# Kernel tuning notes

Measured on AMD Instinct MI355X. Metric: run time of the kernel, lower is better.

The kernel has to match this reference:

```python
import jax, jax.numpy as jnp
import numpy as np
from jax import lax

WINDOW_SIZE = 11
CHANNEL = 3
SIGMA = 1.5


def _build_window():
    # 1D gaussian, normalized, then outer product -> (C, 1, k, k) depthwise kernel
    coords = jnp.arange(WINDOW_SIZE, dtype=jnp.float32) - WINDOW_SIZE // 2
    g = jnp.exp(-coords ** 2 / (2.0 * SIGMA ** 2))
    g = g / g.sum()
    w2d = jnp.outer(g, g)  # (k, k)
    return jnp.broadcast_to(w2d[None, None], (CHANNEL, 1, WINDOW_SIZE, WINDOW_SIZE))


def _dwconv(x, w):
    pad = WINDOW_SIZE // 2
    return lax.conv_general_dilated(
        x, w,
        window_strides=(1, 1),
        padding=[(pad, pad), (pad, pad)],
        dimension_numbers=("NCHW", "OIHW", "NCHW"),
        feature_group_count=CHANNEL,
    )


def setup_inputs() -> dict:
    key = jax.random.key(0)
    k1, k2 = jax.random.split(key)
    pred = jax.random.uniform(k1, (16, 3, 512, 512), dtype=jnp.float32)
    target = jax.random.uniform(k2, (16, 3, 512, 512), dtype=jnp.float32)
    return {"pred": pred, "target": target}


def reference(pred, target):
    C1, C2 = 0.01 ** 2, 0.03 ** 2
    w = _build_window().astype(pred.dtype)

    mu_x = _dwconv(pred, w)
    mu_y = _dwconv(target, w)
    mu_x_sq = mu_x * mu_x
    mu_y_sq = mu_y * mu_y
    mu_xy = mu_x * mu_y

    sg_x = _dwconv(pred * pred, w) - mu_x_sq
    sg_y = _dwconv(target * target, w) - mu_y_sq
    sg_xy = _dwconv(pred * target, w) - mu_xy

    ssim_map = ((2.0 * mu_xy + C1) * (2.0 * sg_xy + C2)) / (
        (mu_x_sq + mu_y_sq + C1) * (sg_x + sg_y + C2)
    )
    return 1.0 - ssim_map.mean()
```

## Files before the change

### kernel.cpp

```cpp
#include <hip/hip_runtime.h>


namespace {
constexpr int IMG   = 512;
constexpr int NCH   = 48;
constexpr int TW    = 64;
constexpr int TH    = 32;
constexpr int WR    = 44;
constexpr int WC    = 80;
constexpr int SLOTS = WC / 4;
constexpr int TSLOT = WR * SLOTS;
constexpr int NSL   = 2 * TSLOT;
constexpr int TPX   = IMG / TW;
constexpr int TPY   = IMG / TH;
constexpr int NBLK  = TPX * TPY * NCH;
constexpr int NPART = NBLK * 4;
constexpr int RS    = 48;
constexpr int SXN   = WR * WC;

constexpr float Wf[11] = {
    0.00102838f, 0.00759876f, 0.03600077f, 0.10936069f, 0.21300554f,
    0.26601172f,
    0.21300554f, 0.10936069f, 0.03600077f, 0.00759876f, 0.00102838f };

constexpr float band_wc(int d) {
    return (d >= 0 && d < 11) ? Wf[d] : 0.f;
}

constexpr unsigned short f2h(float f) {
    if (f == 0.f) return 0;
    unsigned u = __builtin_bit_cast(unsigned, f);
    int  he = int((u >> 23) & 0xff) - 127 + 15;
    unsigned hm   = (u & 0x7fffff) >> 13;
    unsigned rest = u & 0x1fff;
    if (rest > 0x1000 || (rest == 0x1000 && (hm & 1))) ++hm;
    return (unsigned short)((unsigned(he) << 10) + hm);
}

struct Tabs { unsigned short a[64][8]; unsigned short b[64][8]; };
constexpr Tabs build_tabs() {
    Tabs t{};
    for (int lane = 0; lane < 64; ++lane) {
        const int nr = lane & 15, quad = lane >> 4;
        for (int jj = 0; jj < 8; ++jj) {
            const int k = quad * 8 + jj;
            t.a[lane][jj] = f2h(band_wc(k - nr));
            t.b[lane][jj] = f2h(band_wc(k - nr - 3));
        }
    }
    return t;
}
}

__device__ __constant__ __align__(16) Tabs g_tabs = build_tabs();

typedef _Float16 half8 __attribute__((ext_vector_type(8)));
typedef _Float16 half4v __attribute__((ext_vector_type(4)));
typedef _Float16 h2 __attribute__((ext_vector_type(2)));
typedef float float4v __attribute__((ext_vector_type(4)));
typedef float float2v __attribute__((ext_vector_type(2)));

__device__ inline h2 pk(float a, float b) {
    auto v = __builtin_amdgcn_cvt_pkrtz(a, b);
    h2 r;
    __builtin_memcpy(&r, &v, sizeof(r));
    return r;
}

union H8 { half8 v; h2 p[4]; };

__device__ __forceinline__ void gl2l(const float* g, void* l) {
    __builtin_amdgcn_global_load_lds(
        (const __attribute__((address_space(1))) unsigned int*)g,
        (__attribute__((address_space(3))) unsigned int*)l, 16, 0, 0);
}

__global__ __launch_bounds__(256, 4) void ssim_tile_kernel(
    const float* __restrict__ pred, const float* __restrict__ tgt,
    float* __restrict__ partial)
{
    __shared__ __align__(16) float sx[2 * SXN];
    __shared__ __align__(16) _Float16 sc[4][2][16][RS];

    const int t    = threadIdx.x;
    const int w    = t >> 6;
    const int lane = t & 63;
    const int nr   = lane & 15;
    const int quad = lane >> 4;

    const int bid  = blockIdx.x;
    const int img  = bid >> 7;
    const int tile = bid & 127;
    const int tx   = (tile & 7) * TW;
    const int ty   = (tile >> 3) * TH;

    const float* __restrict__ p = pred + (size_t)img * (IMG * IMG);
    const float* __restrict__ q = tgt  + (size_t)img * (IMG * IMG);

    #pragma unroll
    for (int i = 0; i < 7; ++i) {
        const int j = i * 4 + w;
        const int L = j * 64 + lane;
        if (L < NSL) {
            const int tens = (L >= TSLOT) ? 1 : 0;
            const int Lt   = L - tens * TSLOT;
            const int row  = Lt / SLOTS;
            const int sp   = Lt - row * SLOTS;
            int sl = sp - (row & 7);
            if (sl < 0) sl += SLOTS;
            const int gy   = min(max(ty - 5 + row, 0), IMG - 1);
            const int gx   = min(max(tx - 8 + 4 * sl, 0), IMG - 4);
            const float* src = (tens ? q : p) + gy * IMG + gx;
            gl2l(src, (char*)sx + (size_t)j * 1024);
        }
    }
    __syncthreads();

    const half8 Aband = *(const half8*)(g_tabs.a[lane]);
    const half8 Bband = *(const half8*)(g_tabs.b[lane]);
    const float4v zf = {0.f, 0.f, 0.f, 0.f};
    const half8 z8 = {};

    constexpr float C1 = 1e-4f, C2 = 9e-4f;
    const float2v C1v = {C1, C1};
    const float2v C2v = {C2, C2};
    const float2v K12 = {C1 + C2, C1 + C2};
    float2v lsum2 = {0.f, 0.f};

    {
        const int c = w;
        const bool okc_ = ((unsigned)(tx + 16 * c - 8 + 8 * quad)
                           <= (unsigned)(IMG - 8));

        half8 fx[3], fy[3];
        #pragma unroll
        for (int s = 0; s < 3; ++s) {
            const int row  = 16 * s + nr;
            const int rowr = min(row, WR - 1);
            const bool ok  = okc_ && (row < WR) &&
                             ((unsigned)(ty - 5 + row) < (unsigned)IMG);
            const int sl0 = 4 * c + 2 * quad;
            const int r7  = rowr & 7;
            int pos0 = sl0 + r7;     if (pos0 >= SLOTS) pos0 -= SLOTS;
            int pos1 = sl0 + 1 + r7; if (pos1 >= SLOTS) pos1 -= SLOTS;
            const float* b0 = sx + rowr * WC;
            const float* b1 = b0 + SXN;
            float4 xA = *(const float4*)(b0 + 4 * pos0);
            float4 xB = *(const float4*)(b0 + 4 * pos1);
            float4 yA = *(const float4*)(b1 + 4 * pos0);
            float4 yB = *(const float4*)(b1 + 4 * pos1);
            H8 ax, ay;
            ax.p[0] = pk(xA.x, xA.y); ax.p[1] = pk(xA.z, xA.w);
            ax.p[2] = pk(xB.x, xB.y); ax.p[3] = pk(xB.z, xB.w);
            ay.p[0] = pk(yA.x, yA.y); ay.p[1] = pk(yA.z, yA.w);
            ay.p[2] = pk(yB.x, yB.y); ay.p[3] = pk(yB.z, yB.w);
            if (!ok) { ax.v = z8; ay.v = z8; }
            fx[s] = ax.v;
            fy[s] = ay.v;
        }

        auto hw = [&](int slot, int s, float4v d) {
            h2 lo = pk(d[0], d[1]);
            h2 hi = pk(d[2], d[3]);
            half4v hh = {lo[0], lo[1], hi[0], hi[1]};
            *(half4v*)&sc[w][slot][nr][16 * s + 4 * quad] = hh;
        };
        auto rdv = [&](int slot, int pb) -> half8 {
            return *(const half8*)&sc[w][slot][nr][pb + 8 * quad];
        };
        #define HMA(a) __builtin_amdgcn_mfma_f32_16x16x32_f16((a), Bband, zf, 0, 0, 0)
        #define VMA(b) __builtin_amdgcn_mfma_f32_16x16x32_f16(Aband, (b), zf, 0, 0, 0)

        float4v a0[5], a1[5];
        #pragma unroll
        for (int s = 0; s < 3; ++s) { hw(0, s, HMA(fx[s])); hw(1, s, HMA(fy[s])); }
        a0[0] = VMA(rdv(0, 0));  a1[0] = VMA(rdv(0, 16));
        a0[1] = VMA(rdv(1, 0));  a1[1] = VMA(rdv(1, 16));
        #pragma unroll
        for (int s = 0; s < 3; ++s) { hw(0, s, HMA(fx[s] * fx[s])); hw(1, s, HMA(fy[s] * fy[s])); }
        a0[2] = VMA(rdv(0, 0));  a1[2] = VMA(rdv(0, 16));
        a0[3] = VMA(rdv(1, 0));  a1[3] = VMA(rdv(1, 16));
        #pragma unroll
        for (int s = 0; s < 3; ++s) { hw(0, s, HMA(fx[s] * fy[s])); }
        a0[4] = VMA(rdv(0, 0));  a1[4] = VMA(rdv(0, 16));

        #pragma unroll
        for (int v = 0; v < 2; ++v) {
            const float4v* A = v ? a1 : a0;
            #pragma unroll
            for (int h = 0; h < 2; ++h) {
                float2v mx  = {A[0][2*h], A[0][2*h+1]};
                float2v my  = {A[1][2*h], A[1][2*h+1]};
                float2v ex2 = {A[2][2*h], A[2][2*h+1]};
                float2v ey2 = {A[3][2*h], A[3][2*h+1]};
                float2v exy = {A[4][2*h], A[4][2*h+1]};
                float2v P  = mx * my;
                float2v U  = mx * mx + my * my + C1v;
                float2v n1 = 2.f * P + C1v;
                float2v n2 = 2.f * (exy - P) + C2v;
                float2v num = n1 * n2;
                float2v e1 = (ex2 + ey2) - U + K12;
                float2v den = U * e1;
                float2v r = {__builtin_amdgcn_rcpf(den.x),
                             __builtin_amdgcn_rcpf(den.y)};
                lsum2 += num * r;
            }
        }
        #undef HMA
        #undef VMA
    }

    float lsum = lsum2.x + lsum2.y;
    #pragma unroll
    for (int off = 32; off > 0; off >>= 1)
        lsum += __shfl_down(lsum, off, 64);
    if (lane == 0) partial[(bid << 2) + w] = lsum;
}

__global__ __launch_bounds__(1024) void ssim_finish(
    const float* __restrict__ partial, float* __restrict__ out)
{
    __shared__ float wred[16];
    const int t = threadIdx.x;
    float s = 0.f;
    #pragma unroll
    for (int i = 0; i < NPART / 1024; ++i)
        s += partial[t + i * 1024];
    #pragma unroll
    for (int off = 32; off > 0; off >>= 1)
        s += __shfl_down(s, off, 64);
    if ((t & 63) == 0) wred[t >> 6] = s;
    __syncthreads();
    if (t == 0) {
        float acc = 0.f;
        #pragma unroll
        for (int i = 0; i < 16; ++i) acc += wred[i];
        out[0] = 1.f - acc * (1.f / (float)((long long)NCH * IMG * IMG));
    }
}

extern "C" void kernel_launch(void* const* d_in, const int* in_sizes, int n_in,
                              void* d_out, int out_size, void* d_ws, size_t ws_size,
                              hipStream_t stream)
{
    const float* pred = (const float*)d_in[0];
    const float* tgt  = (const float*)d_in[1];
    float* out     = (float*)d_out;
    float* partial = (float*)d_ws;

    ssim_tile_kernel<<<NBLK, 256, 0, stream>>>(pred, tgt, partial);
    ssim_finish<<<1, 1024, 0, stream>>>(partial, out);
}
```

Before: 127.8 us.

## Process four tiles per block with double-buffered async LDS staging

Each block now walks a vertical strip of four 64x32 tiles instead of one. While one LDS buffer is being computed, the global-to-LDS loads for the next tile go into a second buffer, synchronised with explicit vmcnt waits and barriers. This is meant to hide global load latency behind MFMA work and to cut block-launch overhead. The scratch buffer becomes a single slot reused in sequence, which serialises the horizontal and vertical passes. Doubled LDS use and the lowered launch bound cut occupancy, and halo rows are still reloaded for every tile.

```diff
diff --git a/kernel.cpp b/kernel.cpp
--- a/kernel.cpp
+++ b/kernel.cpp
@@ -6,14 +6,15 @@
 constexpr int NCH   = 48;
 constexpr int TW    = 64;
 constexpr int TH    = 32;
+constexpr int NT    = 4;
 constexpr int WR    = 44;
 constexpr int WC    = 80;
 constexpr int SLOTS = WC / 4;
 constexpr int TSLOT = WR * SLOTS;
 constexpr int NSL   = 2 * TSLOT;
 constexpr int TPX   = IMG / TW;
-constexpr int TPY   = IMG / TH;
-constexpr int NBLK  = TPX * TPY * NCH;
+constexpr int NSTRIP= IMG / (TH * NT);
+constexpr int NBLK  = TPX * NSTRIP * NCH;
 constexpr int NPART = NBLK * 4;
 constexpr int RS    = 48;
 constexpr int SXN   = WR * WC;
@@ -75,12 +76,12 @@
         (__attribute__((address_space(3))) unsigned int*)l, 16, 0, 0);
 }
 
-__global__ __launch_bounds__(256, 4) void ssim_tile_kernel(
+__global__ __launch_bounds__(256, 2) void ssim_tile_kernel(
     const float* __restrict__ pred, const float* __restrict__ tgt,
     float* __restrict__ partial)
 {
-    __shared__ __align__(16) float sx[2 * SXN];
-    __shared__ __align__(16) _Float16 sc[4][2][16][RS];
+    __shared__ __align__(16) float sx[2][2 * SXN];
+    __shared__ __align__(16) _Float16 sc[4][16][RS];
 
     const int t    = threadIdx.x;
     const int w    = t >> 6;
@@ -89,46 +90,50 @@
     const int quad = lane >> 4;
 
     const int bid  = blockIdx.x;
-    const int img  = bid >> 7;
-    const int tile = bid & 127;
+    const int img  = bid >> 5;
+    const int tile = bid & 31;
     const int tx   = (tile & 7) * TW;
-    const int ty   = (tile >> 3) * TH;
+    const int ty0  = (tile >> 3) * (TH * NT);
 
     const float* __restrict__ p = pred + (size_t)img * (IMG * IMG);
     const float* __restrict__ q = tgt  + (size_t)img * (IMG * IMG);
 
-    #pragma unroll
-    for (int i = 0; i < 7; ++i) {
-        const int j = i * 4 + w;
-        const int L = j * 64 + lane;
-        if (L < NSL) {
-            const int tens = (L >= TSLOT) ? 1 : 0;
-            const int Lt   = L - tens * TSLOT;
-            const int row  = Lt / SLOTS;
-            const int sp   = Lt - row * SLOTS;
-            int sl = sp - (row & 7);
-            if (sl < 0) sl += SLOTS;
-            const int gy   = min(max(ty - 5 + row, 0), IMG - 1);
-            const int gx   = min(max(tx - 8 + 4 * sl, 0), IMG - 4);
-            const float* src = (tens ? q : p) + gy * IMG + gx;
-            gl2l(src, (char*)sx + (size_t)j * 1024);
-        }
-    }
-    __syncthreads();
-
     const half8 Aband = *(const half8*)(g_tabs.a[lane]);
     const half8 Bband = *(const half8*)(g_tabs.b[lane]);
+    asm volatile("s_waitcnt vmcnt(0)" ::: "memory");
+
     const float4v zf = {0.f, 0.f, 0.f, 0.f};
     const half8 z8 = {};
-
     constexpr float C1 = 1e-4f, C2 = 9e-4f;
     const float2v C1v = {C1, C1};
     const float2v C2v = {C2, C2};
     const float2v K12 = {C1 + C2, C1 + C2};
     float2v lsum2 = {0.f, 0.f};
 
-    {
-        const int c = w;
+    auto STAGE = [&](int it, int buf) {
+        const int ty = ty0 + TH * it;
+        #pragma unroll
+        for (int i = 0; i < 7; ++i) {
+            const int j = i * 4 + w;
+            const int L = j * 64 + lane;
+            if (L < NSL) {
+                const int tens = (L >= TSLOT) ? 1 : 0;
+                const int Lt   = L - tens * TSLOT;
+                const int row  = Lt / SLOTS;
+                const int sp   = Lt - row * SLOTS;
+                int sl = sp - (row & 7);
+                if (sl < 0) sl += SLOTS;
+                const int gy   = min(max(ty - 5 + row, 0), IMG - 1);
+                const int gx   = min(max(tx - 8 + 4 * sl, 0), IMG - 4);
+                const float* src = (tens ? q : p) + gy * IMG + gx;
+                gl2l(src, (char*)sx[buf] + (size_t)j * 1024);
+            }
+        }
+    };
+
+    auto COMPUTE = [&](int it, int buf) {
+        const int ty = ty0 + TH * it;
+        const int c  = w;
         const bool okc_ = ((unsigned)(tx + 16 * c - 8 + 8 * quad)
                            <= (unsigned)(IMG - 8));
 
@@ -143,7 +148,7 @@
             const int r7  = rowr & 7;
             int pos0 = sl0 + r7;     if (pos0 >= SLOTS) pos0 -= SLOTS;
             int pos1 = sl0 + 1 + r7; if (pos1 >= SLOTS) pos1 -= SLOTS;
-            const float* b0 = sx + rowr * WC;
+            const float* b0 = sx[buf] + rowr * WC;
             const float* b1 = b0 + SXN;
             float4 xA = *(const float4*)(b0 + 4 * pos0);
             float4 xB = *(const float4*)(b0 + 4 * pos1);
@@ -159,30 +164,35 @@
             fy[s] = ay.v;
         }
 
-        auto hw = [&](int slot, int s, float4v d) {
+        auto hw = [&](int s, float4v d) {
             h2 lo = pk(d[0], d[1]);
             h2 hi = pk(d[2], d[3]);
             half4v hh = {lo[0], lo[1], hi[0], hi[1]};
-            *(half4v*)&sc[w][slot][nr][16 * s + 4 * quad] = hh;
+            *(half4v*)&sc[w][nr][16 * s + 4 * quad] = hh;
         };
-        auto rdv = [&](int slot, int pb) -> half8 {
-            return *(const half8*)&sc[w][slot][nr][pb + 8 * quad];
+        auto rdv = [&](int pb) -> half8 {
+            return *(const half8*)&sc[w][nr][pb + 8 * quad];
         };
         #define HMA(a) __builtin_amdgcn_mfma_f32_16x16x32_f16((a), Bband, zf, 0, 0, 0)
         #define VMA(b) __builtin_amdgcn_mfma_f32_16x16x32_f16(Aband, (b), zf, 0, 0, 0)
 
         float4v a0[5], a1[5];
         #pragma unroll
-        for (int s = 0; s < 3; ++s) { hw(0, s, HMA(fx[s])); hw(1, s, HMA(fy[s])); }
-        a0[0] = VMA(rdv(0, 0));  a1[0] = VMA(rdv(0, 16));
-        a0[1] = VMA(rdv(1, 0));  a1[1] = VMA(rdv(1, 16));
-        #pragma unroll
-        for (int s = 0; s < 3; ++s) { hw(0, s, HMA(fx[s] * fx[s])); hw(1, s, HMA(fy[s] * fy[s])); }
-        a0[2] = VMA(rdv(0, 0));  a1[2] = VMA(rdv(0, 16));
-        a0[3] = VMA(rdv(1, 0));  a1[3] = VMA(rdv(1, 16));
-        #pragma unroll
-        for (int s = 0; s < 3; ++s) { hw(0, s, HMA(fx[s] * fy[s])); }
-        a0[4] = VMA(rdv(0, 0));  a1[4] = VMA(rdv(0, 16));
+        for (int f = 0; f < 5; ++f) {
+            #pragma unroll
+            for (int s = 0; s < 3; ++s) {
+                half8 prod = (f == 0) ? fx[s]
+                           : (f == 1) ? fy[s]
+                           : (f == 2) ? fx[s] * fx[s]
+                           : (f == 3) ? fy[s] * fy[s]
+                                      : fx[s] * fy[s];
+                hw(s, HMA(prod));
+            }
+            a0[f] = VMA(rdv(0));
+            a1[f] = VMA(rdv(16));
+        }
+        #undef HMA
+        #undef VMA
 
         #pragma unroll
         for (int v = 0; v < 2; ++v) {
@@ -206,8 +216,21 @@
                 lsum2 += num * r;
             }
         }
-        #undef HMA
-        #undef VMA
+    };
+
+    STAGE(0, 0);
+    #pragma unroll 1
+    for (int it = 0; it < NT; ++it) {
+        if (it < NT - 1) {
+            STAGE(it + 1, (it + 1) & 1);
+            asm volatile("s_waitcnt vmcnt(7)" ::: "memory");
+        } else {
+            asm volatile("s_waitcnt vmcnt(0)" ::: "memory");
+        }
+        __builtin_amdgcn_sched_barrier(0);
+        __builtin_amdgcn_s_barrier();
+        COMPUTE(it, it & 1);
+        __builtin_amdgcn_s_barrier();
     }
 
     float lsum = lsum2.x + lsum2.y;
```

Result: slower. 136.5 us (+6.7%).

## Stage input tiles as fp16 in LDS via register loads instead of direct global-to-LDS

Applied to the files above, without the earlier changes.

Replaces the async global_load_lds staging of fp32 tiles with per-thread float4 global loads that are converted to fp16 in registers and stored to a half-sized LDS buffer. The fragment reads then become a single half8 load per tensor per row instead of two float4 loads plus conversions. The LDS footprint shrinks, so the launch bound is raised to 5 blocks per SIMD and the scratch row stride changes. The trade-off is that the async direct-to-LDS path is lost: loads now pass through VGPRs and need conversion before the barrier.

```diff
diff --git a/kernel.cpp b/kernel.cpp
--- a/kernel.cpp
+++ b/kernel.cpp
@@ -8,16 +8,13 @@
 constexpr int TH    = 32;
 constexpr int WR    = 44;
 constexpr int WC    = 80;
-constexpr int SLOTS = WC / 4;
-constexpr int TSLOT = WR * SLOTS;
-constexpr int NSL   = 2 * TSLOT;
+constexpr int SLOTS = WC / 8;
+constexpr int NU    = 2 * WR * SLOTS;
 constexpr int TPX   = IMG / TW;
 constexpr int TPY   = IMG / TH;
 constexpr int NBLK  = TPX * TPY * NCH;
 constexpr int NPART = NBLK * 4;
-constexpr int RS    = 48;
-constexpr int SXN   = WR * WC;
-
+constexpr int RS    = 56;
 constexpr float Wf[11] = {
     0.00102838f, 0.00759876f, 0.03600077f, 0.10936069f, 0.21300554f,
     0.26601172f,
@@ -69,17 +66,11 @@
 
 union H8 { half8 v; h2 p[4]; };
 
-__device__ __forceinline__ void gl2l(const float* g, void* l) {
-    __builtin_amdgcn_global_load_lds(
-        (const __attribute__((address_space(1))) unsigned int*)g,
-        (__attribute__((address_space(3))) unsigned int*)l, 16, 0, 0);
-}
-
-__global__ __launch_bounds__(256, 4) void ssim_tile_kernel(
+__global__ __launch_bounds__(256, 5) void ssim_tile_kernel(
     const float* __restrict__ pred, const float* __restrict__ tgt,
     float* __restrict__ partial)
 {
-    __shared__ __align__(16) float sx[2 * SXN];
+    __shared__ __align__(16) _Float16 wf[2][WR][SLOTS * 8];
     __shared__ __align__(16) _Float16 sc[4][2][16][RS];
 
     const int t    = threadIdx.x;
@@ -98,20 +89,24 @@
     const float* __restrict__ q = tgt  + (size_t)img * (IMG * IMG);
 
     #pragma unroll
-    for (int i = 0; i < 7; ++i) {
-        const int j = i * 4 + w;
-        const int L = j * 64 + lane;
-        if (L < NSL) {
-            const int tens = (L >= TSLOT) ? 1 : 0;
-            const int Lt   = L - tens * TSLOT;
-            const int row  = Lt / SLOTS;
-            const int sp   = Lt - row * SLOTS;
-            int sl = sp - (row & 7);
+    for (int k = 0; k < 4; ++k) {
+        const int u = t + k * 256;
+        if (u < NU) {
+            const int tens = (u >= NU / 2) ? 1 : 0;
+            const int v    = u - tens * (NU / 2);
+            const int row  = v / SLOTS;
+            const int pos  = v - row * SLOTS;
+            int sl = pos - (row & 7);
             if (sl < 0) sl += SLOTS;
-            const int gy   = min(max(ty - 5 + row, 0), IMG - 1);
-            const int gx   = min(max(tx - 8 + 4 * sl, 0), IMG - 4);
+            const int gy = min(max(ty - 5 + row, 0), IMG - 1);
+            const int gx = min(max(tx - 8 + 8 * sl, 0), IMG - 8);
             const float* src = (tens ? q : p) + gy * IMG + gx;
-            gl2l(src, (char*)sx + (size_t)j * 1024);
+            float4 a = *(const float4*)src;
+            float4 b = *(const float4*)(src + 4);
+            H8 h;
+            h.p[0] = pk(a.x, a.y); h.p[1] = pk(a.z, a.w);
+            h.p[2] = pk(b.x, b.y); h.p[3] = pk(b.z, b.w);
+            *(half8*)&wf[tens][row][pos * 8] = h.v;
         }
     }
     __syncthreads();
@@ -139,24 +134,14 @@
             const int rowr = min(row, WR - 1);
             const bool ok  = okc_ && (row < WR) &&
                              ((unsigned)(ty - 5 + row) < (unsigned)IMG);
-            const int sl0 = 4 * c + 2 * quad;
-            const int r7  = rowr & 7;
-            int pos0 = sl0 + r7;     if (pos0 >= SLOTS) pos0 -= SLOTS;
-            int pos1 = sl0 + 1 + r7; if (pos1 >= SLOTS) pos1 -= SLOTS;
-            const float* b0 = sx + rowr * WC;
-            const float* b1 = b0 + SXN;
-            float4 xA = *(const float4*)(b0 + 4 * pos0);
-            float4 xB = *(const float4*)(b0 + 4 * pos1);
-            float4 yA = *(const float4*)(b1 + 4 * pos0);
-            float4 yB = *(const float4*)(b1 + 4 * pos1);
-            H8 ax, ay;
-            ax.p[0] = pk(xA.x, xA.y); ax.p[1] = pk(xA.z, xA.w);
-            ax.p[2] = pk(xB.x, xB.y); ax.p[3] = pk(xB.z, xB.w);
-            ay.p[0] = pk(yA.x, yA.y); ay.p[1] = pk(yA.z, yA.w);
-            ay.p[2] = pk(yB.x, yB.y); ay.p[3] = pk(yB.z, yB.w);
-            if (!ok) { ax.v = z8; ay.v = z8; }
-            fx[s] = ax.v;
-            fy[s] = ay.v;
+            const int sl = 2 * c + quad;
+            int pos = sl + (rowr & 7);
+            if (pos >= SLOTS) pos -= SLOTS;
+            half8 ax = *(const half8*)&wf[0][rowr][pos * 8];
+            half8 ay = *(const half8*)&wf[1][rowr][pos * 8];
+            if (!ok) { ax = z8; ay = z8; }
+            fx[s] = ax;
+            fy[s] = ay;
         }
 
         auto hw = [&](int slot, int s, float4v d) {
@@ -183,6 +168,8 @@
         #pragma unroll
         for (int s = 0; s < 3; ++s) { hw(0, s, HMA(fx[s] * fy[s])); }
         a0[4] = VMA(rdv(0, 0));  a1[4] = VMA(rdv(0, 16));
+        #undef HMA
+        #undef VMA
 
         #pragma unroll
         for (int v = 0; v < 2; ++v) {
@@ -206,8 +193,6 @@
                 lsum2 += num * r;
             }
         }
-        #undef HMA
-        #undef VMA
     }
 
     float lsum = lsum2.x + lsum2.y;
```

After: 130.3 us. No clear change (+2.0%).
